# Optimization experiments

Hardware: AMD Instinct MI355X
Metric: run time of the kernel (lower is better)

The kernel has to match this reference:

```python
import jax, jax.numpy as jnp
import numpy as np

B, S, H, NH = 2, 2048, 2048, 16
DH = H // NH


def setup_inputs() -> dict:
    key = jax.random.key(0)
    ks = jax.random.split(key, 9)
    scale = 1.0 / np.sqrt(H)
    inp = {
        "hidden_state": jax.random.normal(ks[0], (B, S, H), dtype=jnp.float32),
        "Wq": jax.random.normal(ks[1], (H, H), dtype=jnp.float32) * scale,
        "bq": jnp.zeros((H,), dtype=jnp.float32),
        "Wk": jax.random.normal(ks[2], (H, H), dtype=jnp.float32) * scale,
        "bk": jnp.zeros((H,), dtype=jnp.float32),
        "Wv": jax.random.normal(ks[3], (H, H), dtype=jnp.float32) * scale,
        "bv": jnp.zeros((H,), dtype=jnp.float32),
        "Wo": jax.random.normal(ks[4], (H, H), dtype=jnp.float32) * scale,
        "bo": jnp.zeros((H,), dtype=jnp.float32),
    }
    # additive causal mask: 0 on/below diagonal, large negative above
    neg = jnp.float32(-1e9)
    tri = jnp.tril(jnp.ones((S, S), dtype=bool))
    inp["causal_mask"] = jnp.where(tri, 0.0, neg)[None, None, :, :]
    return inp


def reference(hidden_state, Wq, bq, Wk, bk, Wv, bv, Wo, bo, causal_mask):
    def split_heads(x):  # [B,S,H] -> [B,NH,S,DH]
        return x.reshape(B, S, NH, DH).transpose(0, 2, 1, 3)

    q = split_heads(hidden_state @ Wq + bq)
    k = split_heads(hidden_state @ Wk + bk)
    v = split_heads(hidden_state @ Wv + bv)

    scores = jnp.einsum("bhqd,bhkd->bhqk", q, k) / jnp.sqrt(jnp.float32(DH))
    scores = scores + causal_mask
    probs = jax.nn.softmax(scores, axis=-1)
    out = jnp.einsum("bhqk,bhkd->bhqd", probs, v)  # [B,NH,S,DH]
    out = out.transpose(0, 2, 1, 3).reshape(B, S, H)
    return out @ Wo + bo
```

## Files before the change

kernel.cpp:

```cpp
#include <hip/hip_runtime.h>
#include <cstdint>

typedef __attribute__((ext_vector_type(4))) float f32x4;
typedef __attribute__((ext_vector_type(8))) __bf16 bf16x8;
typedef __attribute__((ext_vector_type(4))) unsigned short u16x4;
typedef __attribute__((ext_vector_type(4))) float fvec4;

#define DEV __device__ __forceinline__
#define MFMA16(a, b, c) __builtin_amdgcn_mfma_f32_16x16x32_bf16((a), (b), (c), 0, 0, 0)

DEV unsigned short f2bf(float f) {
  union { float f; uint32_t u; } c; c.f = f;
  uint32_t u = c.u;
  return (unsigned short)((u + 0x7FFFu + ((u >> 16) & 1u)) >> 16);
}

DEV void gll16(const void* g, void* l) {
  __builtin_amdgcn_global_load_lds(
      (const __attribute__((address_space(1))) void*)(uintptr_t)g,
      (__attribute__((address_space(3))) void*)(uint32_t)(uintptr_t)l,
      16, 0, 0);
}

__global__ void cvt_bf16(const float* __restrict__ src, unsigned short* __restrict__ dst) {
  int i = (blockIdx.x * 256 + threadIdx.x) * 4;
  fvec4 v = *(const fvec4*)(src + i);
  u16x4 o;
  o[0] = f2bf(v[0]); o[1] = f2bf(v[1]); o[2] = f2bf(v[2]); o[3] = f2bf(v[3]);
  *(u16x4*)(dst + i) = o;
}

__global__ void transpose_cvt4(const float* __restrict__ W0, const float* __restrict__ W1,
                               const float* __restrict__ W2, const float* __restrict__ W3,
                               unsigned short* __restrict__ Dqkv, unsigned short* __restrict__ Do) {
  __shared__ float t[32][33];
  const float* W = blockIdx.z == 0 ? W0 : blockIdx.z == 1 ? W1 : blockIdx.z == 2 ? W2 : W3;
  unsigned short* WT = blockIdx.z < 3 ? Dqkv + (size_t)blockIdx.z * 2048 * 2048 : Do;
  int n0 = blockIdx.x * 32, k0 = blockIdx.y * 32;
  int x = threadIdx.x, y = threadIdx.y;
  #pragma unroll
  for (int i = 0; i < 32; i += 8)
    t[y + i][x] = W[(size_t)(k0 + y + i) * 2048 + n0 + x];
  __syncthreads();
  #pragma unroll
  for (int i = 0; i < 32; i += 8)
    WT[(size_t)(n0 + y + i) * 2048 + k0 + x] = f2bf(t[x][y + i]);
}

constexpr float QSC = 0.08838834764831845f * 1.4426950408889634f;

template <int MODE>
__global__ __launch_bounds__(256, 2) void gemm128(
    const unsigned short* __restrict__ A,
    const unsigned short* __restrict__ Bt,
    const float* __restrict__ b0, const float* __restrict__ b1,
    const float* __restrict__ b2,
    void* __restrict__ o0, void* __restrict__ o1, void* __restrict__ o2) {
  __shared__ unsigned short As[128 * 64];
  __shared__ unsigned short Bs[128 * 64];
  const int n0 = blockIdx.x * 128, m0 = blockIdx.y * 128;
  const int tid = threadIdx.x;
  const int wave = tid >> 6, lid = tid & 63;
  const int l16 = lid & 15, lq = lid >> 4;
  const int wm = (wave >> 1) * 64, wn = (wave & 1) * 64;

  const int srow = lid >> 3;
  const int sgrp = (lid & 7) ^ srow;

  f32x4 acc[4][4] = {};

  for (int k0 = 0; k0 < 2048; k0 += 64) {
    #pragma unroll
    for (int i = 0; i < 4; ++i) {
      const int t = wave * 4 + i;
      const int r = t * 8 + srow;
      gll16(A + (size_t)(m0 + r) * 2048 + k0 + sgrp * 8, (char*)As + t * 1024 + lid * 16);
      gll16(Bt + (size_t)(n0 + r) * 2048 + k0 + sgrp * 8, (char*)Bs + t * 1024 + lid * 16);
    }
    __syncthreads();
    #pragma unroll
    for (int kk = 0; kk < 2; ++kk) {
      const int G = kk * 4 + lq;
      bf16x8 af[4], bfr[4];
      #pragma unroll
      for (int i = 0; i < 4; ++i)
        af[i] = *(const bf16x8*)(As + (wm + i * 16 + l16) * 64 + ((G ^ (l16 & 7)) << 3));
      #pragma unroll
      for (int j = 0; j < 4; ++j)
        bfr[j] = *(const bf16x8*)(Bs + (wn + j * 16 + l16) * 64 + ((G ^ (l16 & 7)) << 3));
      #pragma unroll
      for (int i = 0; i < 4; ++i)
        #pragma unroll
        for (int j = 0; j < 4; ++j)
          acc[i][j] = MFMA16(af[i], bfr[j], acc[i][j]);
    }
    __syncthreads();
  }

  #pragma unroll
  for (int j = 0; j < 4; ++j) {
    const int c = n0 + wn + j * 16 + l16;
    if (MODE == 1) {
      const int which = c >> 11;
      const int hd = c & 2047;
      const int h = hd >> 7, d = hd & 127;
      const float* bp = which == 0 ? b0 : which == 1 ? b1 : b2;
      const float bv = bp[hd];
      if (which == 2) {
        #pragma unroll
        for (int i = 0; i < 4; ++i) {
          const int row0 = m0 + wm + i * 16 + lq * 4;
          const int bb = row0 >> 11, s0 = row0 & 2047;
          u16x4 pv;
          #pragma unroll
          for (int r = 0; r < 4; ++r) pv[r] = f2bf(acc[i][j][r] + bv);
          *(u16x4*)((unsigned short*)o2 + ((size_t)((bb * 16 + h) * 128 + d)) * 2048 + s0) = pv;
        }
      } else {
        const float sc = which == 0 ? QSC : 1.0f;
        unsigned short* op = which == 0 ? (unsigned short*)o0 : (unsigned short*)o1;
        #pragma unroll
        for (int i = 0; i < 4; ++i) {
          #pragma unroll
          for (int r = 0; r < 4; ++r) {
            const int row = m0 + wm + i * 16 + lq * 4 + r;
            const int bb = row >> 11, s = row & 2047;
            op[(size_t)((bb * 16 + h) * 2048 + s) * 128 + d] = f2bf((acc[i][j][r] + bv) * sc);
          }
        }
      }
    } else {
      const float bv = b0[c];
      #pragma unroll
      for (int i = 0; i < 4; ++i)
        #pragma unroll
        for (int r = 0; r < 4; ++r) {
          const int row = m0 + wm + i * 16 + lq * 4 + r;
          ((float*)o0)[(size_t)row * 2048 + c] = acc[i][j][r] + bv;
        }
    }
  }
}

__global__ __launch_bounds__(256, 4) void attn(
    const unsigned short* __restrict__ Q,
    const unsigned short* __restrict__ K,
    const unsigned short* __restrict__ Vt,
    unsigned short* __restrict__ ctx) {
  __shared__ unsigned short Ks[64 * 128];
  __shared__ unsigned short Vts[128 * 64];
  __shared__ unsigned short Ps[64 * 64];

  const int jq = 31 - (int)blockIdx.x;
  const int q0 = jq * 64;
  const int bh = blockIdx.y;
  const int b = bh >> 4, h = bh & 15;
  const unsigned short* Qh = Q + (size_t)bh * 2048 * 128;
  const unsigned short* Kh = K + (size_t)bh * 2048 * 128;
  const unsigned short* Vth = Vt + (size_t)bh * 128 * 2048;

  const int tid = threadIdx.x;
  const int wave = tid >> 6, lid = tid & 63;
  const int l16 = lid & 15, lq = lid >> 4;
  const int wq = wave * 16;
  const int ql = wq + l16;
  const int qrow = q0 + ql;
  const int sw = 2 * (l16 & 7);

  bf16x8 qf[4];
  #pragma unroll
  for (int kc = 0; kc < 4; ++kc)
    qf[kc] = *(const bf16x8*)(Qh + (size_t)qrow * 128 + kc * 32 + lq * 8);

  float m_i = -1e30f, l_i = 0.f;
  f32x4 acc[8] = {};

  for (int jt = 0; jt <= jq; ++jt) {
    const int k0 = jt * 64;
    #pragma unroll
    for (int ii = 0; ii < 4; ++ii) {
      const int t = wave * 4 + ii;
      const int r = t * 4 + lq;
      const int g = l16 ^ (r & 15);
      gll16(Kh + (size_t)(k0 + r) * 128 + g * 8, (char*)Ks + t * 1024 + lid * 16);
    }
    #pragma unroll
    for (int ii = 0; ii < 4; ++ii) {
      const int t = wave * 4 + ii;
      const int d = t * 8 + (lid >> 3);
      const int g = (lid & 7) ^ (d & 7);
      gll16(Vth + (size_t)d * 2048 + k0 + g * 8, (char*)Vts + t * 1024 + lid * 16);
    }
    __syncthreads();

    f32x4 sacc[4] = {};
    #pragma unroll
    for (int kc = 0; kc < 4; ++kc) {
      #pragma unroll
      for (int km = 0; km < 4; ++km) {
        bf16x8 af = *(const bf16x8*)(Ks + (km * 16 + l16) * 128 + (((kc * 4 + lq) ^ l16) << 3));
        sacc[km] = MFMA16(af, qf[kc], sacc[km]);
      }
    }

    if (jt == jq) {
      #pragma unroll
      for (int km = 0; km < 4; ++km)
        #pragma unroll
        for (int r = 0; r < 4; ++r)
          if (k0 + km * 16 + lq * 4 + r > qrow) sacc[km][r] = -1e30f;
    }

    float tmax = -1e30f;
    #pragma unroll
    for (int km = 0; km < 4; ++km)
      #pragma unroll
      for (int r = 0; r < 4; ++r) tmax = fmaxf(tmax, sacc[km][r]);
    tmax = fmaxf(tmax, __shfl_xor(tmax, 16));
    tmax = fmaxf(tmax, __shfl_xor(tmax, 32));

    const float mnew = fmaxf(m_i, tmax);
    const float alpha = exp2f(m_i - mnew);
    m_i = mnew;

    float ps = 0.f;
    u16x4 pk[4];
    #pragma unroll
    for (int km = 0; km < 4; ++km) {
      #pragma unroll
      for (int r = 0; r < 4; ++r) {
        const float p = exp2f(sacc[km][r] - mnew);
        ps += p;
        pk[km][r] = f2bf(p);
      }
    }
    ps += __shfl_xor(ps, 16);
    ps += __shfl_xor(ps, 32);
    l_i = l_i * alpha + ps;
    #pragma unroll
    for (int dm = 0; dm < 8; ++dm) acc[dm] *= alpha;

    #pragma unroll
    for (int km = 0; km < 4; ++km)
      *(u16x4*)(Ps + ql * 64 + ((((km * 4) + lq) ^ sw) << 2)) = pk[km];

    #pragma unroll
    for (int kc = 0; kc < 2; ++kc) {
      const int G = kc * 4 + lq;
      const int pg = (kc * 8 + 2 * lq) ^ sw;
      bf16x8 pf = *(const bf16x8*)(Ps + ql * 64 + (pg << 2));
      #pragma unroll
      for (int dm = 0; dm < 8; ++dm) {
        bf16x8 vf = *(const bf16x8*)(Vts + (dm * 16 + l16) * 64 + ((G ^ (l16 & 7)) << 3));
        acc[dm] = MFMA16(vf, pf, acc[dm]);
      }
    }
    __syncthreads();
  }

  const float inv = 1.f / l_i;
  const size_t base = ((size_t)(b * 2048 + qrow)) * 2048 + h * 128;
  #pragma unroll
  for (int dm = 0; dm < 8; ++dm) {
    u16x4 o;
    #pragma unroll
    for (int r = 0; r < 4; ++r) o[r] = f2bf(acc[dm][r] * inv);
    *(u16x4*)(ctx + base + dm * 16 + lq * 4) = o;
  }
}

extern "C" void kernel_launch(void* const* d_in, const int* in_sizes, int n_in,
                              void* d_out, int out_size, void* d_ws, size_t ws_size,
                              hipStream_t stream) {
  const float* hs = (const float*)d_in[0];
  const float* Wq = (const float*)d_in[1];
  const float* bq = (const float*)d_in[2];
  const float* Wk = (const float*)d_in[3];
  const float* bk = (const float*)d_in[4];
  const float* Wv = (const float*)d_in[5];
  const float* bv = (const float*)d_in[6];
  const float* Wo = (const float*)d_in[7];
  const float* bo = (const float*)d_in[8];
  float* out = (float*)d_out;

  char* ws = (char*)d_ws;
  unsigned short* hsb   = (unsigned short*)(ws);
  unsigned short* wqkvt = (unsigned short*)(ws + (16 << 20));
  unsigned short* wot   = (unsigned short*)(ws + (40 << 20));
  unsigned short* Qb    = (unsigned short*)(ws + (48 << 20));
  unsigned short* Kb    = (unsigned short*)(ws + (64 << 20));
  unsigned short* Vtb   = (unsigned short*)(ws + (80 << 20));
  unsigned short* ctx   = (unsigned short*)(ws + (96 << 20));

  cvt_bf16<<<dim3(8192), dim3(256), 0, stream>>>(hs, hsb);
  transpose_cvt4<<<dim3(64, 64, 4), dim3(32, 8), 0, stream>>>(Wq, Wk, Wv, Wo, wqkvt, wot);

  gemm128<1><<<dim3(48, 32), 256, 0, stream>>>(hsb, wqkvt, bq, bk, bv,
                                               (void*)Qb, (void*)Kb, (void*)Vtb);
  attn<<<dim3(32, 32), 256, 0, stream>>>(Qb, Kb, Vtb, ctx);
  gemm128<0><<<dim3(16, 32), 256, 0, stream>>>(ctx, wot, bo, nullptr, nullptr,
                                               (void*)out, nullptr, nullptr);
}
```

Measured before the change: 410.5 us.

## Use 32x32 MFMA with 128-row query tiles in attention; swizzle GEMM block order

The attention kernel moves from 16x16x32 to 32x32x16 bf16 MFMA, each wave now owning 32 query rows, so a block covers 128 queries. This halves the number of blocks and doubles the reuse of each K/V tile. Causal load balance comes from reversing the block order for the first half of the batch-heads, and P is packed to bf16 with a perm-based rounding helper. The GEMMs switch to a 1D grid with a grouped M/N mapping meant to improve L2 reuse. The changes cost lower occupancy (launch bounds 2) and more registers, and the new pack2 rounding is round-half-up rather than round-to-nearest-even.

```diff
diff --git a/kernel.cpp b/kernel.cpp
--- a/kernel.cpp
+++ b/kernel.cpp
@@ -2,17 +2,26 @@
 #include <cstdint>
 
 typedef __attribute__((ext_vector_type(4))) float f32x4;
+typedef __attribute__((ext_vector_type(16))) float f32x16;
 typedef __attribute__((ext_vector_type(8))) __bf16 bf16x8;
 typedef __attribute__((ext_vector_type(4))) unsigned short u16x4;
+typedef __attribute__((ext_vector_type(2))) unsigned int u32x2;
 typedef __attribute__((ext_vector_type(4))) float fvec4;
 
 #define DEV __device__ __forceinline__
 #define MFMA16(a, b, c) __builtin_amdgcn_mfma_f32_16x16x32_bf16((a), (b), (c), 0, 0, 0)
+#define MFMA32(a, b, c) __builtin_amdgcn_mfma_f32_32x32x16_bf16((a), (b), (c), 0, 0, 0)
 
 DEV unsigned short f2bf(float f) {
   union { float f; uint32_t u; } c; c.f = f;
   uint32_t u = c.u;
   return (unsigned short)((u + 0x7FFFu + ((u >> 16) & 1u)) >> 16);
+}
+
+DEV unsigned int pack2(float lo, float hi) {
+  union { float f; uint32_t u; } a, b;
+  a.f = lo; b.f = hi;
+  return __builtin_amdgcn_perm(b.u + 0x8000u, a.u + 0x8000u, 0x07060302u);
 }
 
 DEV void gll16(const void* g, void* l) {
@@ -58,7 +67,9 @@
     void* __restrict__ o0, void* __restrict__ o1, void* __restrict__ o2) {
   __shared__ unsigned short As[128 * 64];
   __shared__ unsigned short Bs[128 * 64];
-  const int n0 = blockIdx.x * 128, m0 = blockIdx.y * 128;
+  const int id = blockIdx.x;
+  const int m0 = (((id & 7) << 2) | ((id >> 3) & 3)) * 128;
+  const int n0 = (id >> 5) * 128;
   const int tid = threadIdx.x;
   const int wave = tid >> 6, lid = tid & 63;
   const int l16 = lid & 15, lq = lid >> 4;
@@ -142,18 +153,18 @@
   }
 }
 
-__global__ __launch_bounds__(256, 4) void attn(
+__global__ __launch_bounds__(256, 2) void attn(
     const unsigned short* __restrict__ Q,
     const unsigned short* __restrict__ K,
     const unsigned short* __restrict__ Vt,
     unsigned short* __restrict__ ctx) {
   __shared__ unsigned short Ks[64 * 128];
   __shared__ unsigned short Vts[128 * 64];
-  __shared__ unsigned short Ps[64 * 64];
-
-  const int jq = 31 - (int)blockIdx.x;
-  const int q0 = jq * 64;
+  __shared__ unsigned short Ps[4 * 32 * 64];
+
   const int bh = blockIdx.y;
+  const int jq = (bh < 16) ? (15 - (int)blockIdx.x) : (int)blockIdx.x;
+  const int q0 = jq * 128;
   const int b = bh >> 4, h = bh & 15;
   const unsigned short* Qh = Q + (size_t)bh * 2048 * 128;
   const unsigned short* Kh = K + (size_t)bh * 2048 * 128;
@@ -161,27 +172,27 @@
 
   const int tid = threadIdx.x;
   const int wave = tid >> 6, lid = tid & 63;
-  const int l16 = lid & 15, lq = lid >> 4;
-  const int wq = wave * 16;
-  const int ql = wq + l16;
-  const int qrow = q0 + ql;
-  const int sw = 2 * (l16 & 7);
-
-  bf16x8 qf[4];
-  #pragma unroll
-  for (int kc = 0; kc < 4; ++kc)
-    qf[kc] = *(const bf16x8*)(Qh + (size_t)qrow * 128 + kc * 32 + lq * 8);
+  const int l32 = lid & 31, half = lid >> 5;
+  const int qrow = q0 + wave * 32 + l32;
+  unsigned short* Pw = Ps + wave * 2048 + l32 * 64;
+  const int qsw = l32 & 7;
+
+  bf16x8 qf[8];
+  #pragma unroll
+  for (int ds = 0; ds < 8; ++ds)
+    qf[ds] = *(const bf16x8*)(Qh + (size_t)qrow * 128 + ds * 16 + half * 8);
 
   float m_i = -1e30f, l_i = 0.f;
-  f32x4 acc[8] = {};
-
-  for (int jt = 0; jt <= jq; ++jt) {
+  f32x16 acc[4] = {};
+
+  const int ntiles = 2 * jq + 2;
+  for (int jt = 0; jt < ntiles; ++jt) {
     const int k0 = jt * 64;
     #pragma unroll
     for (int ii = 0; ii < 4; ++ii) {
       const int t = wave * 4 + ii;
-      const int r = t * 4 + lq;
-      const int g = l16 ^ (r & 15);
+      const int r = t * 4 + (lid >> 4);
+      const int g = (lid & 15) ^ (r & 15);
       gll16(Kh + (size_t)(k0 + r) * 128 + g * 8, (char*)Ks + t * 1024 + lid * 16);
     }
     #pragma unroll
@@ -193,30 +204,32 @@
     }
     __syncthreads();
 
-    f32x4 sacc[4] = {};
-    #pragma unroll
-    for (int kc = 0; kc < 4; ++kc) {
-      #pragma unroll
-      for (int km = 0; km < 4; ++km) {
-        bf16x8 af = *(const bf16x8*)(Ks + (km * 16 + l16) * 128 + (((kc * 4 + lq) ^ l16) << 3));
-        sacc[km] = MFMA16(af, qf[kc], sacc[km]);
-      }
-    }
-
-    if (jt == jq) {
-      #pragma unroll
-      for (int km = 0; km < 4; ++km)
-        #pragma unroll
-        for (int r = 0; r < 4; ++r)
-          if (k0 + km * 16 + lq * 4 + r > qrow) sacc[km][r] = -1e30f;
+    f32x16 sacc[2] = {};
+    #pragma unroll
+    for (int ds = 0; ds < 8; ++ds) {
+      #pragma unroll
+      for (int mb = 0; mb < 2; ++mb) {
+        const int kr = mb * 32 + l32;
+        bf16x8 af = *(const bf16x8*)(Ks + kr * 128 + (((ds * 2 + half) ^ (kr & 15)) << 3));
+        sacc[mb] = MFMA32(af, qf[ds], sacc[mb]);
+      }
+    }
+
+    if (jt >= 2 * jq) {
+      #pragma unroll
+      for (int mb = 0; mb < 2; ++mb)
+        #pragma unroll
+        for (int i = 0; i < 16; ++i) {
+          const int kg = k0 + mb * 32 + (i & 3) + 8 * (i >> 2) + 4 * half;
+          if (kg > qrow) sacc[mb][i] = -1e30f;
+        }
     }
 
     float tmax = -1e30f;
     #pragma unroll
-    for (int km = 0; km < 4; ++km)
-      #pragma unroll
-      for (int r = 0; r < 4; ++r) tmax = fmaxf(tmax, sacc[km][r]);
-    tmax = fmaxf(tmax, __shfl_xor(tmax, 16));
+    for (int mb = 0; mb < 2; ++mb)
+      #pragma unroll
+      for (int i = 0; i < 16; ++i) tmax = fmaxf(tmax, sacc[mb][i]);
     tmax = fmaxf(tmax, __shfl_xor(tmax, 32));
 
     const float mnew = fmaxf(m_i, tmax);
@@ -224,35 +237,36 @@
     m_i = mnew;
 
     float ps = 0.f;
-    u16x4 pk[4];
-    #pragma unroll
-    for (int km = 0; km < 4; ++km) {
-      #pragma unroll
-      for (int r = 0; r < 4; ++r) {
-        const float p = exp2f(sacc[km][r] - mnew);
-        ps += p;
-        pk[km][r] = f2bf(p);
-      }
-    }
-    ps += __shfl_xor(ps, 16);
+    #pragma unroll
+    for (int mb = 0; mb < 2; ++mb) {
+      #pragma unroll
+      for (int i = 0; i < 16; ++i) {
+        sacc[mb][i] = exp2f(sacc[mb][i] - mnew);
+        ps += sacc[mb][i];
+      }
+      #pragma unroll
+      for (int u = 0; u < 4; ++u) {
+        u32x2 w;
+        w[0] = pack2(sacc[mb][4 * u], sacc[mb][4 * u + 1]);
+        w[1] = pack2(sacc[mb][4 * u + 2], sacc[mb][4 * u + 3]);
+        *(u32x2*)(Pw + (((u + mb * 4) ^ qsw) << 3) + half * 4) = w;
+      }
+    }
     ps += __shfl_xor(ps, 32);
     l_i = l_i * alpha + ps;
     #pragma unroll
-    for (int dm = 0; dm < 8; ++dm) acc[dm] *= alpha;
-
-    #pragma unroll
-    for (int km = 0; km < 4; ++km)
-      *(u16x4*)(Ps + ql * 64 + ((((km * 4) + lq) ^ sw) << 2)) = pk[km];
-
-    #pragma unroll
-    for (int kc = 0; kc < 2; ++kc) {
-      const int G = kc * 4 + lq;
-      const int pg = (kc * 8 + 2 * lq) ^ sw;
-      bf16x8 pf = *(const bf16x8*)(Ps + ql * 64 + (pg << 2));
-      #pragma unroll
-      for (int dm = 0; dm < 8; ++dm) {
-        bf16x8 vf = *(const bf16x8*)(Vts + (dm * 16 + l16) * 64 + ((G ^ (l16 & 7)) << 3));
-        acc[dm] = MFMA16(vf, pf, acc[dm]);
+    for (int db = 0; db < 4; ++db)
+      #pragma unroll
+      for (int i = 0; i < 16; ++i) acc[db][i] *= alpha;
+
+    #pragma unroll
+    for (int ks = 0; ks < 4; ++ks) {
+      bf16x8 pf = *(const bf16x8*)(Pw + (((ks * 2 + half) ^ qsw) << 3));
+      #pragma unroll
+      for (int db = 0; db < 4; ++db) {
+        const int d = db * 32 + l32;
+        bf16x8 vf = *(const bf16x8*)(Vts + d * 64 + (((ks * 2 + half) ^ (d & 7)) << 3));
+        acc[db] = MFMA32(vf, pf, acc[db]);
       }
     }
     __syncthreads();
@@ -261,11 +275,14 @@
   const float inv = 1.f / l_i;
   const size_t base = ((size_t)(b * 2048 + qrow)) * 2048 + h * 128;
   #pragma unroll
-  for (int dm = 0; dm < 8; ++dm) {
-    u16x4 o;
-    #pragma unroll
-    for (int r = 0; r < 4; ++r) o[r] = f2bf(acc[dm][r] * inv);
-    *(u16x4*)(ctx + base + dm * 16 + lq * 4) = o;
+  for (int db = 0; db < 4; ++db) {
+    #pragma unroll
+    for (int u = 0; u < 4; ++u) {
+      u32x2 w;
+      w[0] = pack2(acc[db][4 * u] * inv, acc[db][4 * u + 1] * inv);
+      w[1] = pack2(acc[db][4 * u + 2] * inv, acc[db][4 * u + 3] * inv);
+      *(u32x2*)(ctx + base + db * 32 + 8 * u + 4 * half) = w;
+    }
   }
 }
 
@@ -295,9 +312,9 @@
   cvt_bf16<<<dim3(8192), dim3(256), 0, stream>>>(hs, hsb);
   transpose_cvt4<<<dim3(64, 64, 4), dim3(32, 8), 0, stream>>>(Wq, Wk, Wv, Wo, wqkvt, wot);
 
-  gemm128<1><<<dim3(48, 32), 256, 0, stream>>>(hsb, wqkvt, bq, bk, bv,
-                                               (void*)Qb, (void*)Kb, (void*)Vtb);
-  attn<<<dim3(32, 32), 256, 0, stream>>>(Qb, Kb, Vtb, ctx);
-  gemm128<0><<<dim3(16, 32), 256, 0, stream>>>(ctx, wot, bo, nullptr, nullptr,
-                                               (void*)out, nullptr, nullptr);
-}
+  gemm128<1><<<dim3(1536), 256, 0, stream>>>(hsb, wqkvt, bq, bk, bv,
+                                             (void*)Qb, (void*)Kb, (void*)Vtb);
+  attn<<<dim3(16, 32), 256, 0, stream>>>(Qb, Kb, Vtb, ctx);
+  gemm128<0><<<dim3(512), 256, 0, stream>>>(ctx, wot, bo, nullptr, nullptr,
+                                            (void*)out, nullptr, nullptr);
+}
```

Result: faster. 380.1 us (-7.4%).
